# Optimization experiments

Hardware: AMD Instinct MI355X
Metric: run time of the kernel (lower is better)

The kernel has to match this reference:

```python
import jax, jax.numpy as jnp
import numpy as np

NUM_HEADS = 16
D_MODEL = 1024
HEAD_DIM = D_MODEL // NUM_HEADS
EMB = 1024
B, L = 2, 2048


def setup_inputs() -> dict:
    key = jax.random.key(0)
    k1, k2, k3 = jax.random.split(key, 3)
    scale_in = 1.0 / np.sqrt(EMB)
    scale_out = 1.0 / np.sqrt(D_MODEL)
    return {
        "x": jax.random.normal(k1, (B, L, EMB), dtype=jnp.float32),
        "W_qkv": jax.random.normal(k2, (EMB, 3 * D_MODEL), dtype=jnp.float32) * scale_in,
        "b_qkv": jnp.zeros((3 * D_MODEL,), dtype=jnp.float32),
        "W_out": jax.random.normal(k3, (D_MODEL, EMB), dtype=jnp.float32) * scale_out,
        "b_out": jnp.zeros((EMB,), dtype=jnp.float32),
    }


def reference(x, W_qkv, b_qkv, W_out, b_out):
    Bn, Ln, _ = x.shape
    qkv = x @ W_qkv + b_qkv  # [B, L, 3*d_model]
    q = qkv[:, :, :D_MODEL].reshape(Bn, Ln, NUM_HEADS, HEAD_DIM)
    k = qkv[:, :, D_MODEL:2 * D_MODEL].reshape(Bn, Ln, NUM_HEADS, HEAD_DIM)
    v = qkv[:, :, 2 * D_MODEL:].reshape(Bn, Ln, NUM_HEADS, HEAD_DIM)
    scores = jnp.einsum('bqhd,bkhd->bhqk', q, k)  # [B, H, L, L]
    attn = jax.nn.softmax(scores / jnp.sqrt(jnp.float32(HEAD_DIM)), axis=-1)
    out = jnp.einsum('bhqk,bkhd->bqhd', attn, v).reshape(Bn, Ln, D_MODEL)
    return out @ W_out + b_out
```

## Files before the change

kernel.cpp:

```cpp
#include <hip/hip_runtime.h>
#include <stdint.h>

#define B_   2
#define L_   2048
#define H_   16
#define D_   64
#define EMB_ 1024
#define DM_  1024
#define N3_  3072
#define TOK_ 4096

typedef unsigned short u16;
typedef unsigned int u32;
typedef __attribute__((ext_vector_type(4))) float f32x4;
typedef __attribute__((ext_vector_type(8))) short s16x8;
typedef __attribute__((ext_vector_type(4))) short s16x4;
typedef __attribute__((ext_vector_type(4))) u32 u32x4;
typedef __attribute__((ext_vector_type(2))) u32 u32x2;
typedef __attribute__((ext_vector_type(4))) u16 u16x4;

#define MFMA(a,b,c) __builtin_amdgcn_mfma_f32_16x16x32_bf16(a,b,c,0,0,0)

#if defined(__has_builtin)
#if __has_builtin(__builtin_amdgcn_mfma_f32_16x16x16bf16_1k)
#define MFMA16(a,b,c) __builtin_amdgcn_mfma_f32_16x16x16bf16_1k(a,b,c,0,0,0)
#endif
#endif
#ifndef MFMA16
static __device__ __forceinline__ f32x4 mfma16_asm(s16x4 a, s16x4 b, f32x4 c) {
  asm volatile("v_mfma_f32_16x16x16_bf16 %0, %1, %2, %0"
               : "+v"(c) : "v"(a), "v"(b));
  return c;
}
#define MFMA16(a,b,c) mfma16_asm(a,b,c)
#endif

#define AS1 __attribute__((address_space(1)))
#define AS3 __attribute__((address_space(3)))
#define GLLDS(g, l) __builtin_amdgcn_global_load_lds( \
    (const AS1 u32*)(const void*)(g), (AS3 u32*)(void*)(l), 16, 0, 0)

#define QSCALE 0.18033688011f

static __device__ __forceinline__ u16 f2bf(float f) {
  u32 u = __builtin_bit_cast(u32, f);
  return (u16)((u + 0x8000u) >> 16);
}

static __device__ __forceinline__ float bf2f(u16 v) {
  u32 u = ((u32)v) << 16;
  return __builtin_bit_cast(float, u);
}

static __device__ __forceinline__ u16 f2h(float f) {
  _Float16 h = (_Float16)f;
  return __builtin_bit_cast(u16, h);
}

static __device__ __forceinline__ float h2f(u16 v) {
  _Float16 h = __builtin_bit_cast(_Float16, v);
  return (float)h;
}

static __device__ __forceinline__ u32 pack2bf(float a, float b) {
  u32 ua = __builtin_bit_cast(u32, a) + 0x8000u;
  u32 ub = __builtin_bit_cast(u32, b) + 0x8000u;
  return __builtin_amdgcn_perm(ub, ua, 0x07060302u);
}

static __device__ __forceinline__ float fexp2(float x) {
#if __has_builtin(__builtin_amdgcn_exp2f)
  return __builtin_amdgcn_exp2f(x);
#else
  float r;
  asm("v_exp_f32 %0, %1" : "=v"(r) : "v"(x));
  return r;
#endif
}

__global__ __launch_bounds__(256) void k_prep(
    const float* __restrict__ x,   u16* __restrict__ xb,
    const float* __restrict__ Wq,  u16* __restrict__ wqT,
    const float* __restrict__ Wo,  u16* __restrict__ woT)
{
  const int blk = blockIdx.x, tid = threadIdx.x;
  if (blk < 4096) {
    int i = (blk * 256 + tid) * 4;
    float4 v = *(const float4*)(x + i);
    ushort4 o;
    o.x = f2bf(v.x); o.y = f2bf(v.y); o.z = f2bf(v.z); o.w = f2bf(v.w);
    *(ushort4*)(xb + i) = o;
    return;
  }
  __shared__ float tile[32][33];
  const float* in;
  u16* out;
  int R, C, bx, by;
  if (blk < 4096 + 3072) {
    int t = blk - 4096;
    in = Wq; out = wqT; R = EMB_; C = N3_;
    bx = t % 96; by = t / 96;
  } else {
    int t = blk - 7168;
    in = Wo; out = woT; R = DM_; C = DM_;
    bx = t & 31; by = t >> 5;
  }
  int c0 = bx * 32, r0 = by * 32;
  int tx = tid & 31, ty = tid >> 5;
  #pragma unroll
  for (int i = 0; i < 32; i += 8)
    tile[ty + i][tx] = in[(size_t)(r0 + ty + i) * C + (c0 + tx)];
  __syncthreads();
  int c = tid >> 3, j = tid & 7;
  u16x4 o;
  #pragma unroll
  for (int r = 0; r < 4; ++r)
    o[r] = f2bf(tile[j * 4 + r][c]);
  *(u16x4*)(out + (size_t)(c0 + c) * R + r0 + j * 4) = o;
}

template<int EPI, int BN>
__global__ __launch_bounds__(256, 4) void k_gemm(
    const u16* __restrict__ A, const u16* __restrict__ Bt,
    const float* __restrict__ bias, int M, int N, int K,
    float* __restrict__ Cf,
    u16* __restrict__ Qo, u16* __restrict__ Ko, u16* __restrict__ Vo)
{
  constexpr int NF = BN / 32;
  constexpr int BROWS = (BN == 128) ? 32 : 16;
  const int tid = threadIdx.x;
  const int wave = tid >> 6, lane = tid & 63;
  const int lr = lane & 15, lk = lane >> 4;
  const int wr = wave >> 1, wc = wave & 1;
  const int m0 = blockIdx.y * 128, n0 = blockIdx.x * BN;

  __shared__ u16 As[2][128 * 32];
  __shared__ u16 Bs[2][BN * 32];

  f32x4 acc[4][NF] = {};

  const int srow = wave * 32 + (lane >> 2);
  const int srowB = (BN == 128) ? srow : (wave * 16 + (lane >> 2));
  const int schunk = (lane & 3) * 8;
  const u16* gA = A  + (size_t)(m0 + srow) * K + schunk;
  const u16* gB = Bt + (size_t)(n0 + srowB) * K + schunk;
  const size_t rstep = (size_t)16 * K;
  u16* lA0 = (u16*)As[0] + wave * (32 * 32);
  u16* lA1 = (u16*)As[1] + wave * (32 * 32);
  u16* lB0 = (u16*)Bs[0] + wave * (BROWS * 32);
  u16* lB1 = (u16*)Bs[1] + wave * (BROWS * 32);

  GLLDS(gA,         lA0);
  GLLDS(gA + rstep, lA0 + 16 * 32);
  GLLDS(gB,         lB0);
  if (BN == 128) GLLDS(gB + rstep, lB0 + 16 * 32);

  int buf = 0;
  for (int k0 = 0; k0 < K; k0 += 32, buf ^= 1) {
    __syncthreads();

    if (k0 + 32 < K) {
      u16* dA = buf ? lA0 : lA1;
      u16* dB = buf ? lB0 : lB1;
      GLLDS(gA + k0 + 32,         dA);
      GLLDS(gA + k0 + 32 + rstep, dA + 16 * 32);
      GLLDS(gB + k0 + 32,         dB);
      if (BN == 128) GLLDS(gB + k0 + 32 + rstep, dB + 16 * 32);
    }

    const u16* Ab = (const u16*)As[buf];
    const u16* Bb = (const u16*)Bs[buf];
    s16x8 af[4], bfr[NF];
    #pragma unroll
    for (int mi = 0; mi < 4; ++mi)
      af[mi] = *(const s16x8*)(Ab + (wr * 64 + mi * 16 + lr) * 32 + lk * 8);
    #pragma unroll
    for (int ni = 0; ni < NF; ++ni)
      bfr[ni] = *(const s16x8*)(Bb + (wc * (BN / 2) + ni * 16 + lr) * 32 + lk * 8);
    #pragma unroll
    for (int mi = 0; mi < 4; ++mi)
      #pragma unroll
      for (int ni = 0; ni < NF; ++ni)
        acc[mi][ni] = MFMA(af[mi], bfr[ni], acc[mi][ni]);
  }

  const int mbase = m0 + wr * 64 + lk * 4;
  #pragma unroll
  for (int ni = 0; ni < NF; ++ni) {
    int gn = n0 + wc * (BN / 2) + ni * 16 + lr;
    float bz = bias[gn];
    if (EPI == 1) {
      #pragma unroll
      for (int mi = 0; mi < 4; ++mi)
        #pragma unroll
        for (int r = 0; r < 4; ++r) {
          int gm = mbase + mi * 16 + r;
          Cf[(size_t)gm * N + gn] = acc[mi][ni][r] + bz;
        }
    } else {
      int sec = gn >> 10, cm = gn & 1023;
      int h = cm >> 6, d = cm & 63;
      if (sec == 2) {
        #pragma unroll
        for (int mi = 0; mi < 4; ++mi) {
          int gm0 = mbase + mi * 16;
          int b = gm0 >> 11, l0 = gm0 & 2047;
          int bh = b * H_ + h;
          u16x4 vv;
          #pragma unroll
          for (int r = 0; r < 4; ++r) vv[r] = f2bf(acc[mi][ni][r] + bz);
          *(u16x4*)(Vo + ((size_t)bh * D_ + d) * L_ + l0) = vv;
        }
      } else {
        #pragma unroll
        for (int mi = 0; mi < 4; ++mi)
          #pragma unroll
          for (int r = 0; r < 4; ++r) {
            int gm = mbase + mi * 16 + r;
            float v = acc[mi][ni][r] + bz;
            int b = gm >> 11, l = gm & 2047;
            int bh = b * H_ + h;
            if (sec == 0) Qo[((size_t)bh * L_ + l) * D_ + d] = f2bf(v * QSCALE);
            else          Ko[((size_t)bh * L_ + l) * D_ + d] = f2bf(v);
          }
      }
    }
  }
}

__global__ __launch_bounds__(256, 2) void k_flash(
    const u16* __restrict__ Q, const u16* __restrict__ Kb,
    const u16* __restrict__ Vt,
    u16* __restrict__ O0, u16* __restrict__ O1, float* __restrict__ lpart)
{
  const int tid = threadIdx.x;
  const int wave = tid >> 6, lane = tid & 63;
  const int lr = lane & 15, lk = lane >> 4;
  const int blk = blockIdx.x;
  const int idx = blk >> 3;
  const int bh = (blk & 7) * 4 + (idx >> 4);
  const int rem = idx & 15;
  const int qt = rem >> 1;
  const int half = rem & 1;
  const int tbase = half * 1024;
  const int b = bh >> 4, h = bh & 15;
  const u16* Qh = Q  + (size_t)bh * L_ * D_;
  const u16* Kh = Kb + (size_t)bh * L_ * D_;
  const u16* Vh = Vt + (size_t)bh * D_ * L_;

  __shared__ u16 Ks[2][64 * 64];
  __shared__ u16 Vs[2][64 * 64];

  const int qrow0 = qt * 256 + wave * 64;
  s16x8 qf[4][2];
  #pragma unroll
  for (int g = 0; g < 4; ++g)
    #pragma unroll
    for (int ks = 0; ks < 2; ++ks)
      qf[g][ks] = *(const s16x8*)(Qh + (size_t)(qrow0 + g * 16 + lr) * D_ + ks * 32 + lk * 8);

  f32x4 acco[4][4] = {};
  float lst[4] = {0.f, 0.f, 0.f, 0.f};
  const f32x4 zz = {0.f, 0.f, 0.f, 0.f};

  const int srow0 = wave * 16 + (lane >> 3);
  const int gch8 = (((lane & 7) ^ ((lane >> 3) & 7)) * 8);
  u16* kd0 = (u16*)Ks[0] + wave * (16 * 64);
  u16* kd1 = (u16*)Ks[1] + wave * (16 * 64);
  u16* vd0 = (u16*)Vs[0] + wave * (16 * 64);
  u16* vd1 = (u16*)Vs[1] + wave * (16 * 64);

  const int sx7 = lr & 7;
  const int ck0 = (lk ^ sx7) * 8;
  const int vsub = (lk & 1) * 4;
  const int vx = lk >> 1;

  GLLDS(Kh + (size_t)(tbase + srow0) * 64 + gch8,       kd0);
  GLLDS(Kh + (size_t)(tbase + srow0 + 8) * 64 + gch8,   kd0 + 8 * 64);
  GLLDS(Vh + ((size_t)srow0 * L_ + tbase + gch8),       vd0);
  GLLDS(Vh + ((size_t)(srow0 + 8) * L_ + tbase + gch8), vd0 + 8 * 64);

  int buf = 0;
  const int tend = tbase + 1024;
  for (int t0 = tbase; t0 < tend; t0 += 64, buf ^= 1) {
    __syncthreads();

    if (t0 + 64 < tend) {
      const int tn = t0 + 64;
      u16* kd = buf ? kd0 : kd1;
      u16* vd = buf ? vd0 : vd1;
      GLLDS(Kh + (size_t)(tn + srow0) * 64 + gch8,       kd);
      GLLDS(Kh + (size_t)(tn + srow0 + 8) * 64 + gch8,   kd + 8 * 64);
      GLLDS(Vh + ((size_t)srow0 * L_ + tn + gch8),       vd);
      GLLDS(Vh + ((size_t)(srow0 + 8) * L_ + tn + gch8), vd + 8 * 64);
    }

    const u16* Kbuf = (const u16*)Ks[buf];
    const u16* Vbuf = (const u16*)Vs[buf];
    #pragma unroll
    for (int mi = 0; mi < 4; ++mi) {
      const u16* rp = Kbuf + (mi * 16 + lr) * 64;
      s16x8 kf0 = *(const s16x8*)(rp + ck0);
      s16x8 kf1 = *(const s16x8*)(rp + (ck0 ^ 32));
      const int vofs = ((2 * mi + vx) ^ sx7) * 8 + vsub;
      s16x4 vf[4];
      #pragma unroll
      for (int di = 0; di < 4; ++di)
        vf[di] = *(const s16x4*)(Vbuf + (di * 16 + lr) * 64 + vofs);
      #pragma unroll
      for (int g = 0; g < 4; ++g) {
        f32x4 s = MFMA(kf0, qf[g][0], zz);
        s = MFMA(kf1, qf[g][1], s);
        float p0 = fexp2(s[0]), p1 = fexp2(s[1]);
        float p2 = fexp2(s[2]), p3 = fexp2(s[3]);
        lst[g] += (p0 + p1) + (p2 + p3);
        u32x2 pw = { pack2bf(p0, p1), pack2bf(p2, p3) };
        s16x4 pk = __builtin_bit_cast(s16x4, pw);
        #pragma unroll
        for (int di = 0; di < 4; ++di)
          acco[g][di] = MFMA16(vf[di], pk, acco[g][di]);
      }
    }
  }

  u16* Oh = half ? O1 : O0;
  #pragma unroll
  for (int g = 0; g < 4; ++g) {
    float l = lst[g];
    l += __shfl_xor(l, 16);
    l += __shfl_xor(l, 32);
    const int q = qrow0 + g * 16 + lr;
    if (lk == 0)
      lpart[((size_t)(half << 5) + bh) * L_ + q] = l;
    #pragma unroll
    for (int di = 0; di < 4; ++di) {
      u16x4 o;
      #pragma unroll
      for (int r = 0; r < 4; ++r)
        o[r] = f2h(acco[g][di][r]);
      *(u16x4*)(Oh + (size_t)(b * L_ + q) * DM_ + h * D_ + di * 16 + lk * 4) = o;
    }
  }
}

__global__ __launch_bounds__(256) void k_comb(
    const u16* __restrict__ O0, const u16* __restrict__ O1,
    const float* __restrict__ lpart, u16* __restrict__ AO)
{
  const int row = blockIdx.x;
  const int b = row >> 11, l = row & 2047;
  const int c = threadIdx.x * 4;
  const int h = c >> 6;
  const size_t bhl = (size_t)(b * H_ + h) * L_ + l;
  const float rl = 1.0f / (lpart[bhl] + lpart[(size_t)32 * L_ + bhl]);
  const size_t off = (size_t)row * DM_ + c;
  u16x4 a = *(const u16x4*)(O0 + off);
  u16x4 bb = *(const u16x4*)(O1 + off);
  u16x4 o;
  #pragma unroll
  for (int r = 0; r < 4; ++r)
    o[r] = f2bf((h2f(a[r]) + h2f(bb[r])) * rl);
  *(u16x4*)(AO + off) = o;
}

extern "C" void kernel_launch(void* const* d_in, const int* in_sizes, int n_in,
                              void* d_out, int out_size, void* d_ws, size_t ws_size,
                              hipStream_t stream)
{
  const float* x    = (const float*)d_in[0];
  const float* Wqkv = (const float*)d_in[1];
  const float* bqkv = (const float*)d_in[2];
  const float* Wout = (const float*)d_in[3];
  const float* bout = (const float*)d_in[4];
  float* out = (float*)d_out;

  u16* xb  = (u16*)d_ws;
  u16* wqT = xb  + (size_t)TOK_ * EMB_;
  u16* woT = wqT + (size_t)N3_ * EMB_;
  u16* qb  = woT + (size_t)DM_ * EMB_;
  u16* kb  = qb  + (size_t)B_ * H_ * L_ * D_;
  u16* vt  = kb  + (size_t)B_ * H_ * L_ * D_;
  u16* ao  = vt  + (size_t)B_ * H_ * L_ * D_;
  float* lpart = (float*)wqT;

  k_prep<<<4096 + 3072 + 1024, 256, 0, stream>>>(x, xb, Wqkv, wqT, Wout, woT);
  k_gemm<0, 128><<<dim3(N3_ / 128, TOK_ / 128), 256, 0, stream>>>(
      xb, wqT, bqkv, TOK_, N3_, EMB_, nullptr, qb, kb, vt);
  k_flash<<<512, 256, 0, stream>>>(qb, kb, vt, ao, xb, lpart);
  k_comb<<<TOK_, 256, 0, stream>>>(ao, xb, lpart, ao);
  k_gemm<1, 64><<<dim3(DM_ / 64, TOK_ / 128), 256, 0, stream>>>(
      ao, woT, bout, TOK_, DM_, EMB_, out, nullptr, nullptr, nullptr);
}
```

Baseline: 187.3 us.

## Triple-buffer K/V tiles in flash kernel with partial vmcnt waits

```diff
diff --git a/kernel.cpp b/kernel.cpp
--- a/kernel.cpp
+++ b/kernel.cpp
@@ -228,6 +228,15 @@
   }
 }
 
+#define KSTAGE(kb_, vb_, tn_) do { \
+    u16* kd_ = (u16*)(kb_) + wave * (16 * 64); \
+    u16* vd_ = (u16*)(vb_) + wave * (16 * 64); \
+    GLLDS(Kh + (size_t)((tn_) + srow0) * 64 + gch8,       kd_); \
+    GLLDS(Kh + (size_t)((tn_) + srow0 + 8) * 64 + gch8,   kd_ + 8 * 64); \
+    GLLDS(Vh + ((size_t)srow0 * L_ + (tn_) + gch8),       vd_); \
+    GLLDS(Vh + ((size_t)(srow0 + 8) * L_ + (tn_) + gch8), vd_ + 8 * 64); \
+  } while (0)
+
 __global__ __launch_bounds__(256, 2) void k_flash(
     const u16* __restrict__ Q, const u16* __restrict__ Kb,
     const u16* __restrict__ Vt,
@@ -248,8 +257,8 @@
   const u16* Kh = Kb + (size_t)bh * L_ * D_;
   const u16* Vh = Vt + (size_t)bh * D_ * L_;
 
-  __shared__ u16 Ks[2][64 * 64];
-  __shared__ u16 Vs[2][64 * 64];
+  __shared__ u16 Ks[3][64 * 64];
+  __shared__ u16 Vs[3][64 * 64];
 
   const int qrow0 = qt * 256 + wave * 64;
   s16x8 qf[4][2];
@@ -265,38 +274,28 @@
 
   const int srow0 = wave * 16 + (lane >> 3);
   const int gch8 = (((lane & 7) ^ ((lane >> 3) & 7)) * 8);
-  u16* kd0 = (u16*)Ks[0] + wave * (16 * 64);
-  u16* kd1 = (u16*)Ks[1] + wave * (16 * 64);
-  u16* vd0 = (u16*)Vs[0] + wave * (16 * 64);
-  u16* vd1 = (u16*)Vs[1] + wave * (16 * 64);
 
   const int sx7 = lr & 7;
   const int ck0 = (lk ^ sx7) * 8;
   const int vsub = (lk & 1) * 4;
   const int vx = lk >> 1;
 
-  GLLDS(Kh + (size_t)(tbase + srow0) * 64 + gch8,       kd0);
-  GLLDS(Kh + (size_t)(tbase + srow0 + 8) * 64 + gch8,   kd0 + 8 * 64);
-  GLLDS(Vh + ((size_t)srow0 * L_ + tbase + gch8),       vd0);
-  GLLDS(Vh + ((size_t)(srow0 + 8) * L_ + tbase + gch8), vd0 + 8 * 64);
-
-  int buf = 0;
-  const int tend = tbase + 1024;
-  for (int t0 = tbase; t0 < tend; t0 += 64, buf ^= 1) {
-    __syncthreads();
-
-    if (t0 + 64 < tend) {
-      const int tn = t0 + 64;
-      u16* kd = buf ? kd0 : kd1;
-      u16* vd = buf ? vd0 : vd1;
-      GLLDS(Kh + (size_t)(tn + srow0) * 64 + gch8,       kd);
-      GLLDS(Kh + (size_t)(tn + srow0 + 8) * 64 + gch8,   kd + 8 * 64);
-      GLLDS(Vh + ((size_t)srow0 * L_ + tn + gch8),       vd);
-      GLLDS(Vh + ((size_t)(srow0 + 8) * L_ + tn + gch8), vd + 8 * 64);
-    }
-
-    const u16* Kbuf = (const u16*)Ks[buf];
-    const u16* Vbuf = (const u16*)Vs[buf];
+  KSTAGE(Ks[0], Vs[0], tbase);
+  KSTAGE(Ks[1], Vs[1], tbase + 64);
+
+  int c = 0, n = 1, p = 2;
+  #pragma unroll 1
+  for (int i = 0; i < 16; ++i) {
+    if (i < 15) { asm volatile("s_waitcnt vmcnt(4)" ::: "memory"); }
+    else        { asm volatile("s_waitcnt vmcnt(0)" ::: "memory"); }
+    __builtin_amdgcn_s_barrier();
+    asm volatile("" ::: "memory");
+
+    if (i + 2 < 16)
+      KSTAGE(Ks[p], Vs[p], tbase + (i + 2) * 64);
+
+    const u16* Kbuf = (const u16*)Ks[c];
+    const u16* Vbuf = (const u16*)Vs[c];
     #pragma unroll
     for (int mi = 0; mi < 4; ++mi) {
       const u16* rp = Kbuf + (mi * 16 + lr) * 64;
@@ -321,6 +320,8 @@
           acco[g][di] = MFMA16(vf[di], pk, acco[g][di]);
       }
     }
+
+    int rot = c; c = n; n = p; p = rot;
   }
 
   u16* Oh = half ? O1 : O0;
```

After: 191.9 us. 2.5% more time.
